# Kernel optimization log

Hardware: AMD Instinct MI355X
Metric: run time of the kernel (lower is better)

Reference implementation:

```python
import jax, jax.numpy as jnp
import numpy as np

N_BINS = 15  # matches L2ECELoss(n_bins=15)


def setup_inputs() -> dict:
    key = jax.random.key(0)
    k1, k2 = jax.random.split(key)
    N = 33554432  # 2**25 samples
    confidences = jax.random.uniform(k1, (N,), dtype=jnp.float32)
    accuracies = jax.random.uniform(k2, (N,), dtype=jnp.float32)
    return {"confidences": confidences, "accuracies": accuracies}


def reference(confidences, accuracies):
    # bin_boundaries = linspace(0, 1, n_bins+1); bin b covers (lower_b, upper_b]
    boundaries = jnp.linspace(0.0, 1.0, N_BINS + 1)
    n = confidences.shape[0]
    # conf in (lower, upper]  <=>  searchsorted(boundaries, conf, 'left') - 1 == bin index
    idx = jnp.searchsorted(boundaries, confidences, side="left") - 1
    # conf <= 0 or conf > 1 falls in no bin (original uses strict gt(lower))
    valid = (confidences > 0.0) & (confidences <= 1.0)
    idx_c = jnp.clip(idx, 0, N_BINS - 1)
    w = valid.astype(confidences.dtype)
    # one-pass segment reductions over all bins (replaces the Python loop)
    counts = jax.ops.segment_sum(w, idx_c, num_segments=N_BINS)
    conf_sum = jax.ops.segment_sum(confidences * w, idx_c, num_segments=N_BINS)
    acc_sum = jax.ops.segment_sum(accuracies * w, idx_c, num_segments=N_BINS)
    safe_counts = jnp.maximum(counts, 1.0)
    avg_conf = conf_sum / safe_counts
    avg_acc = acc_sum / safe_counts
    prop_in_bin = counts / n
    per_bin = jnp.square(avg_conf - avg_acc) * prop_in_bin
    ece = jnp.sum(jnp.where(counts > 0, per_bin, 0.0))
    return ece
```

## Files before the change

kernel.cpp:

```cpp
#include <hip/hip_runtime.h>

#define NBINS 15
#define TPB   128
#define GRID  1280
#define NROWS (3 * NBINS)
#define HREC  (NBINS * TPB)

__device__ __forceinline__ void ece_elem(float c, float a,
                                         float4* __restrict__ slot) {
    const float INV15 = 1.0f / 15.0f;
    float t  = c * 15.0f;
    float f0 = truncf(t);
    int   b  = (int)f0;
    b += (c > (f0 + 1.0f) * INV15) ? 1 : 0;
    b -= (c <= f0 * INV15)         ? 1 : 0;
    b = min(max(b, 0), NBINS - 1);
    float w = ((c > 0.0f) && (c <= 1.0f)) ? 1.0f : 0.0f;
    float4 r = slot[b * TPB];
    r.x += w;
    r.y = fmaf(w, c, r.y);
    r.z = fmaf(w, a, r.z);
    slot[b * TPB] = r;
}

__global__ __launch_bounds__(TPB, 2) void ece_partial(const float* __restrict__ conf,
                                                      const float* __restrict__ acc,
                                                      float* __restrict__ ws,
                                                      int N, int slotMode) {
    __shared__ float4 hist4[HREC];
    __shared__ float  wred[2][NROWS];
    const int tid  = threadIdx.x;
    const int lane = tid & 63;
    const int wid  = tid >> 6;

    {
        float4 z = {0.f, 0.f, 0.f, 0.f};
        for (int i = tid; i < HREC; i += TPB) hist4[i] = z;
    }
    __syncthreads();

    float4* slot = &hist4[tid];

    const int gid    = blockIdx.x * TPB + tid;
    const int stride = GRID * TPB;
    const float4* c4 = (const float4*)conf;
    const float4* a4 = (const float4*)acc;
    const int N8 = N >> 3;

    int  p    = gid;
    bool have = p < N8;
    float4 c0, c1, a0, a1;
    if (have) {
        c0 = c4[2 * p]; c1 = c4[2 * p + 1];
        a0 = a4[2 * p]; a1 = a4[2 * p + 1];
    }
    while (have) {
        const int  pn = p + stride;
        const bool hn = pn < N8;
        const int  pl = hn ? pn : p;
        float4 d0 = c4[2 * pl], d1 = c4[2 * pl + 1];
        float4 e0 = a4[2 * pl], e1 = a4[2 * pl + 1];

        ece_elem(c0.x, a0.x, slot);
        ece_elem(c0.y, a0.y, slot);
        ece_elem(c0.z, a0.z, slot);
        ece_elem(c0.w, a0.w, slot);
        ece_elem(c1.x, a1.x, slot);
        ece_elem(c1.y, a1.y, slot);
        ece_elem(c1.z, a1.z, slot);
        ece_elem(c1.w, a1.w, slot);

        c0 = d0; c1 = d1; a0 = e0; a1 = e1;
        p = pn; have = hn;
    }

    for (int i = (N8 << 3) + gid; i < N; i += stride)
        ece_elem(conf[i], acc[i], slot);

    __syncthreads();

    for (int b = 0; b < NBINS; ++b) {
        float4 r = hist4[b * TPB + tid];
        float x = r.x, y = r.y, z = r.z;
        #pragma unroll
        for (int s = 32; s >= 1; s >>= 1) {
            x += __shfl_xor(x, s);
            y += __shfl_xor(y, s);
            z += __shfl_xor(z, s);
        }
        if (lane == 0) {
            wred[wid][b]             = x;
            wred[wid][NBINS + b]     = y;
            wred[wid][2 * NBINS + b] = z;
        }
    }
    __syncthreads();

    if (tid < NROWS) {
        float S = wred[0][tid] + wred[1][tid];
        if (slotMode) ws[tid * GRID + blockIdx.x] = S;
        else          atomicAdd(&ws[tid], S);
    }
}

__global__ __launch_bounds__(1024) void ece_final_slots(const float* __restrict__ ws,
                                                        float* __restrict__ out, int N) {
    __shared__ double red[NROWS];
    const int tid = threadIdx.x, lane = tid & 63, w = tid >> 6;
    for (int r = w; r < NROWS; r += 16) {
        double s = 0.0;
        #pragma unroll 4
        for (int it = 0; it < GRID / 64; ++it)
            s += (double)ws[r * GRID + it * 64 + lane];
        #pragma unroll
        for (int sft = 32; sft >= 1; sft >>= 1) s += __shfl_xor(s, sft);
        if (lane == 0) red[r] = s;
    }
    __syncthreads();
    if (w == 0) {
        double per = 0.0;
        if (lane < NBINS) {
            double cnt = red[lane];
            double cs  = red[NBINS + lane];
            double as  = red[2 * NBINS + lane];
            double safe = cnt > 1.0 ? cnt : 1.0;
            double d = cs / safe - as / safe;
            per = (cnt > 0.0) ? d * d * (cnt / (double)N) : 0.0;
        }
        per += __shfl_down(per, 8);
        per += __shfl_down(per, 4);
        per += __shfl_down(per, 2);
        per += __shfl_down(per, 1);
        if (lane == 0) out[0] = (float)per;
    }
}

__global__ void ece_zero_ws(float* __restrict__ ws) {
    int t = threadIdx.x;
    if (t < NROWS) ws[t] = 0.0f;
}

__global__ void ece_final_atomic(const float* __restrict__ ws,
                                 float* __restrict__ out, int N) {
    int lane = threadIdx.x;
    double per = 0.0;
    if (lane < NBINS) {
        double cnt = (double)ws[lane];
        double cs  = (double)ws[NBINS + lane];
        double as  = (double)ws[2 * NBINS + lane];
        double safe = cnt > 1.0 ? cnt : 1.0;
        double d = cs / safe - as / safe;
        per = (cnt > 0.0) ? d * d * (cnt / (double)N) : 0.0;
    }
    per += __shfl_down(per, 8);
    per += __shfl_down(per, 4);
    per += __shfl_down(per, 2);
    per += __shfl_down(per, 1);
    if (lane == 0) out[0] = (float)per;
}

extern "C" void kernel_launch(void* const* d_in, const int* in_sizes, int n_in,
                              void* d_out, int out_size, void* d_ws, size_t ws_size,
                              hipStream_t stream) {
    const float* conf = (const float*)d_in[0];
    const float* acc  = (const float*)d_in[1];
    float* out = (float*)d_out;
    float* ws  = (float*)d_ws;
    const int N = in_sizes[0];

    const size_t need = (size_t)NROWS * GRID * sizeof(float);
    const int slotMode = (ws_size >= need) ? 1 : 0;

    if (!slotMode) ece_zero_ws<<<1, 64, 0, stream>>>(ws);
    ece_partial<<<GRID, TPB, 0, stream>>>(conf, acc, ws, N, slotMode);
    if (slotMode) ece_final_slots<<<1, 1024, 0, stream>>>(ws, out, N);
    else          ece_final_atomic<<<1, 64, 0, stream>>>(ws, out, N);
}
```

Baseline: 63.57 us.

## Accumulate per-bin conf-acc difference and count, shrink histogram to float2

Instead of separate confidence and accuracy sums, each bin now accumulates the sum of (c - a) and a count. The per-bin term is computed as s1^2/(count*N), which is algebraically equal to the original. Bin assignment is reduced to a plain truncation with no boundary correction steps. The LDS histogram shrinks from float4 to float2, and the grid is doubled with launch bounds raised to 5 blocks per CU for more occupancy. The risks are that bin edges may differ for values right at a boundary, and that the difference-sum loses some precision.

```diff
diff --git a/kernel.cpp b/kernel.cpp
--- a/kernel.cpp
+++ b/kernel.cpp
@@ -2,44 +2,53 @@
 
 #define NBINS 15
 #define TPB   128
-#define GRID  1280
-#define NROWS (3 * NBINS)
+#define GRID  2560
+#define NROWS (2 * NBINS)
 #define HREC  (NBINS * TPB)
 
 __device__ __forceinline__ void ece_elem(float c, float a,
-                                         float4* __restrict__ slot) {
-    const float INV15 = 1.0f / 15.0f;
-    float t  = c * 15.0f;
-    float f0 = truncf(t);
-    int   b  = (int)f0;
-    b += (c > (f0 + 1.0f) * INV15) ? 1 : 0;
-    b -= (c <= f0 * INV15)         ? 1 : 0;
+                                         float2* __restrict__ slot) {
+    float cm = (c <= 1.0f) ? c : 0.0f;
+    int b = (int)truncf(cm * 15.0f);
     b = min(max(b, 0), NBINS - 1);
-    float w = ((c > 0.0f) && (c <= 1.0f)) ? 1.0f : 0.0f;
-    float4 r = slot[b * TPB];
-    r.x += w;
-    r.y = fmaf(w, c, r.y);
-    r.z = fmaf(w, a, r.z);
+    float w  = (cm > 0.0f) ? 1.0f : 0.0f;
+    float wd = w * (c - a);
+    float2 r = slot[b * TPB];
+    r.x += wd;
+    r.y += w;
     slot[b * TPB] = r;
 }
 
-__global__ __launch_bounds__(TPB, 2) void ece_partial(const float* __restrict__ conf,
+__device__ __forceinline__ void ece_batch(const float4& c0, const float4& c1,
+                                          const float4& a0, const float4& a1,
+                                          float2* __restrict__ slot) {
+    ece_elem(c0.x, a0.x, slot);
+    ece_elem(c0.y, a0.y, slot);
+    ece_elem(c0.z, a0.z, slot);
+    ece_elem(c0.w, a0.w, slot);
+    ece_elem(c1.x, a1.x, slot);
+    ece_elem(c1.y, a1.y, slot);
+    ece_elem(c1.z, a1.z, slot);
+    ece_elem(c1.w, a1.w, slot);
+}
+
+__global__ __launch_bounds__(TPB, 5) void ece_partial(const float* __restrict__ conf,
                                                       const float* __restrict__ acc,
                                                       float* __restrict__ ws,
                                                       int N, int slotMode) {
-    __shared__ float4 hist4[HREC];
+    __shared__ float2 hist2[HREC];
     __shared__ float  wred[2][NROWS];
     const int tid  = threadIdx.x;
     const int lane = tid & 63;
     const int wid  = tid >> 6;
 
     {
-        float4 z = {0.f, 0.f, 0.f, 0.f};
-        for (int i = tid; i < HREC; i += TPB) hist4[i] = z;
+        float2 z = {0.f, 0.f};
+        for (int i = tid; i < HREC; i += TPB) hist2[i] = z;
     }
     __syncthreads();
 
-    float4* slot = &hist4[tid];
+    float2* slot = &hist2[tid];
 
     const int gid    = blockIdx.x * TPB + tid;
     const int stride = GRID * TPB;
@@ -61,14 +70,7 @@
         float4 d0 = c4[2 * pl], d1 = c4[2 * pl + 1];
         float4 e0 = a4[2 * pl], e1 = a4[2 * pl + 1];
 
-        ece_elem(c0.x, a0.x, slot);
-        ece_elem(c0.y, a0.y, slot);
-        ece_elem(c0.z, a0.z, slot);
-        ece_elem(c0.w, a0.w, slot);
-        ece_elem(c1.x, a1.x, slot);
-        ece_elem(c1.y, a1.y, slot);
-        ece_elem(c1.z, a1.z, slot);
-        ece_elem(c1.w, a1.w, slot);
+        ece_batch(c0, c1, a0, a1, slot);
 
         c0 = d0; c1 = d1; a0 = e0; a1 = e1;
         p = pn; have = hn;
@@ -80,18 +82,16 @@
     __syncthreads();
 
     for (int b = 0; b < NBINS; ++b) {
-        float4 r = hist4[b * TPB + tid];
-        float x = r.x, y = r.y, z = r.z;
+        float2 r = hist2[b * TPB + tid];
+        float x = r.x, y = r.y;
         #pragma unroll
         for (int s = 32; s >= 1; s >>= 1) {
             x += __shfl_xor(x, s);
             y += __shfl_xor(y, s);
-            z += __shfl_xor(z, s);
         }
         if (lane == 0) {
-            wred[wid][b]             = x;
-            wred[wid][NBINS + b]     = y;
-            wred[wid][2 * NBINS + b] = z;
+            wred[wid][b]         = x;
+            wred[wid][NBINS + b] = y;
         }
     }
     __syncthreads();
@@ -120,12 +120,9 @@
     if (w == 0) {
         double per = 0.0;
         if (lane < NBINS) {
-            double cnt = red[lane];
-            double cs  = red[NBINS + lane];
-            double as  = red[2 * NBINS + lane];
-            double safe = cnt > 1.0 ? cnt : 1.0;
-            double d = cs / safe - as / safe;
-            per = (cnt > 0.0) ? d * d * (cnt / (double)N) : 0.0;
+            double s1 = red[lane];
+            double s2 = red[NBINS + lane];
+            per = (s2 > 0.0) ? (s1 * s1) / (s2 * (double)N) : 0.0;
         }
         per += __shfl_down(per, 8);
         per += __shfl_down(per, 4);
@@ -145,12 +142,9 @@
     int lane = threadIdx.x;
     double per = 0.0;
     if (lane < NBINS) {
-        double cnt = (double)ws[lane];
-        double cs  = (double)ws[NBINS + lane];
-        double as  = (double)ws[2 * NBINS + lane];
-        double safe = cnt > 1.0 ? cnt : 1.0;
-        double d = cs / safe - as / safe;
-        per = (cnt > 0.0) ? d * d * (cnt / (double)N) : 0.0;
+        double s1 = (double)ws[lane];
+        double s2 = (double)ws[NBINS + lane];
+        per = (s2 > 0.0) ? (s1 * s1) / (s2 * (double)N) : 0.0;
     }
     per += __shfl_down(per, 8);
     per += __shfl_down(per, 4);
```

After: 62.73 us. No clear change (-1.3%).
